# Optimization experiments

Hardware: AMD Instinct MI355X
Metric: run time of the kernel (lower is better)

Reference implementation:

```python
import jax, jax.numpy as jnp
import numpy as np

C = 256
D = C // 8  # query/key channels


def setup_inputs() -> dict:
    key = jax.random.key(0)
    ks = jax.random.split(key, 7)
    x = jax.random.normal(ks[0], (4, C, 64, 64), dtype=jnp.float32)
    s1 = 1.0 / np.sqrt(C)
    w1 = jax.random.normal(ks[1], (D, C), dtype=jnp.float32) * s1
    b1 = jax.random.normal(ks[2], (D,), dtype=jnp.float32) * 0.01
    w2 = jax.random.normal(ks[3], (D, C), dtype=jnp.float32) * s1
    b2 = jax.random.normal(ks[4], (D,), dtype=jnp.float32) * 0.01
    w3 = jax.random.normal(ks[5], (C, C), dtype=jnp.float32) * s1
    b3 = jax.random.normal(ks[6], (C,), dtype=jnp.float32) * 0.01
    return {"x": x, "w1": w1, "b1": b1, "w2": w2, "b2": b2, "w3": w3, "b3": b3}


def reference(x, w1, b1, w2, b2, w3, b3):
    B, Cc, W, H = x.shape
    N = W * H
    xf = x.reshape(B, Cc, N)  # [B, C, N] flattened spatial
    # 1x1 convs are per-pixel linear maps over channels
    q = jnp.einsum('dc,bcn->bnd', w1, xf) + b1  # [B, N, D]
    k = jnp.einsum('dc,bcn->bdn', w2, xf) + b2[:, None]  # [B, D, N]
    v = jnp.einsum('oc,bcn->bon', w3, xf) + b3[:, None]  # [B, C, N]
    energy = jnp.einsum('bnd,bdm->bnm', q, k)  # [B, N, N]
    attn = jax.nn.softmax(energy, axis=-1)
    out = jnp.einsum('bcm,bnm->bcn', v, attn)  # bmm(V, attn^T)
    out = out.reshape(B, Cc, W, H) + x
    return out
```

## Files before the change

### kernel.cpp

```cpp
#include <hip/hip_runtime.h>
#include <hip/hip_fp16.h>

typedef _Float16 half8 __attribute__((ext_vector_type(8)));
typedef _Float16 half2v __attribute__((ext_vector_type(2)));
typedef float f32x16 __attribute__((ext_vector_type(16)));
typedef float f32x4v __attribute__((ext_vector_type(4)));

#define MFMA16(A, B, C) __builtin_amdgcn_mfma_f32_32x32x16_f16((A), (B), (C), 0, 0, 0)

__device__ __forceinline__ f32x16 fzero16() {
  f32x16 z;
#pragma unroll
  for (int i = 0; i < 16; ++i) z[i] = 0.0f;
  return z;
}

struct HiLo { _Float16 hi, lo; };
__device__ __forceinline__ HiLo split1(float f) {
  HiLo r;
  r.hi = (_Float16)f;
  r.lo = (_Float16)(f - (float)r.hi);
  return r;
}

__global__ __launch_bounds__(256) void wprep_kernel(
    const float* __restrict__ w1, const float* __restrict__ w2,
    const float* __restrict__ w3,
    _Float16* __restrict__ w1p, _Float16* __restrict__ w2p,
    _Float16* __restrict__ w3p)
{
  const int t = threadIdx.x;
  const int blk = blockIdx.x;
  if (blk < 8) {
    const int cot = blk;
    for (int e = t; e < 8192; e += 256) {
      const int j = e & 7, l = (e >> 3) & 63, cs = e >> 9;
      const int lr = l & 31, h = l >> 5;
      const int row = cot * 32 + lr;
      const int col = cs * 16 + 4 * h + (j & 3) + 8 * (j >> 2);
      const HiLo s = split1(w3[row * 256 + col]);
      const int idx = ((cot * 16 + cs) * 64 + l) * 8 + j;
      w3p[idx] = s.hi;
      w3p[65536 + idx] = s.lo;
    }
  } else {
    for (int e = t; e < 8192; e += 256) {
      const int j = e & 7, l = (e >> 3) & 63, cs = e >> 9;
      const int lr = l & 31, h = l >> 5;
      const int col = cs * 16 + 4 * h + (j & 3) + 8 * (j >> 2);
      const HiLo s1 = split1(w1[lr * 256 + col]);
      const HiLo s2 = split1(w2[lr * 256 + col]);
      const int idx = (cs * 64 + l) * 8 + j;
      w1p[idx] = s1.hi; w1p[8192 + idx] = s1.lo;
      w2p[idx] = s2.hi; w2p[8192 + idx] = s2.lo;
    }
  }
}

__global__ __launch_bounds__(256) void qk_proj_kernel(
    const float* __restrict__ x,
    const _Float16* __restrict__ w1p, const float* __restrict__ b1,
    const _Float16* __restrict__ w2p, const float* __restrict__ b2,
    _Float16* __restrict__ qb, _Float16* __restrict__ kb)
{
  __shared__ f32x4v red[4][2][4][64];
  const int t = threadIdx.x, w = t >> 6, l = t & 63;
  const int lr = l & 31, h = l >> 5;
  const int b = blockIdx.x >> 7;
  const int rt = blockIdx.x & 127;
  const float* xb = x + (size_t)b * 256 * 4096 + rt * 32 + lr;

  f32x16 accq = fzero16(), acck = fzero16();

  for (int cs = w * 4; cs < w * 4 + 4; ++cs) {
    const int c0 = cs * 16 + 4 * h;
    half8 xh, xl;
#pragma unroll
    for (int j = 0; j < 8; ++j) {
      const int c = c0 + (j & 3) + 8 * (j >> 2);
      const HiLo s = split1(xb[(size_t)c * 4096]);
      xh[j] = s.hi; xl[j] = s.lo;
    }
    const half8 w1h = *(const half8*)&w1p[(cs * 64 + l) * 8];
    const half8 w1l = *(const half8*)&w1p[8192 + (cs * 64 + l) * 8];
    const half8 w2h = *(const half8*)&w2p[(cs * 64 + l) * 8];
    const half8 w2l = *(const half8*)&w2p[8192 + (cs * 64 + l) * 8];
    accq = MFMA16(w1h, xh, accq);
    accq = MFMA16(w1h, xl, accq);
    accq = MFMA16(w1l, xh, accq);
    acck = MFMA16(w2h, xh, acck);
    acck = MFMA16(w2h, xl, acck);
    acck = MFMA16(w2l, xh, acck);
  }

#pragma unroll
  for (int i4 = 0; i4 < 4; ++i4) {
    f32x4v q4, k4;
#pragma unroll
    for (int c = 0; c < 4; ++c) { q4[c] = accq[4 * i4 + c]; k4[c] = acck[4 * i4 + c]; }
    red[w][0][i4][l] = q4;
    red[w][1][i4][l] = k4;
  }
  __syncthreads();
  if (w < 2) {
    _Float16* dst = (w == 0) ? qb : kb;
    const float* bias = (w == 0) ? b1 : b2;
    f32x16 tot;
#pragma unroll
    for (int i4 = 0; i4 < 4; ++i4) {
      f32x4v v = red[0][w][i4][l];
      v += red[1][w][i4][l];
      v += red[2][w][i4][l];
      v += red[3][w][i4][l];
#pragma unroll
      for (int c = 0; c < 4; ++c) tot[4 * i4 + c] = v[c];
    }
#pragma unroll
    for (int ds = 0; ds < 2; ++ds) {
      half8 ph;
#pragma unroll
      for (int j = 0; j < 8; ++j) {
        const int d = 16 * ds + 4 * h + (j & 3) + 8 * (j >> 2);
        ph[j] = (_Float16)(tot[8 * ds + j] + bias[d]);
      }
      *(half8*)&dst[((((size_t)b * 128 + rt) * 2 + ds) * 64 + l) * 8] = ph;
    }
  }
}

__global__ __launch_bounds__(256) void v_proj_kernel(
    const float* __restrict__ x, const _Float16* __restrict__ w3p,
    const float* __restrict__ b3, _Float16* __restrict__ vb)
{
  const int t = threadIdx.x, w = t >> 6, l = t & 63;
  const int lr = l & 31, h = l >> 5;
  const int b = blockIdx.x >> 7;
  const int nt = blockIdx.x & 127;
  const float* xb = x + (size_t)b * 256 * 4096 + nt * 32 + lr;
  const int cot0 = w * 2, cot1 = w * 2 + 1;

  f32x16 acc0 = fzero16(), acc1 = fzero16();

  for (int cs = 0; cs < 16; ++cs) {
    const int c0 = cs * 16 + 4 * h;
    half8 xh, xl;
#pragma unroll
    for (int j = 0; j < 8; ++j) {
      const int c = c0 + (j & 3) + 8 * (j >> 2);
      const HiLo s = split1(xb[(size_t)c * 4096]);
      xh[j] = s.hi; xl[j] = s.lo;
    }
    const half8 wh0 = *(const half8*)&w3p[((cot0 * 16 + cs) * 64 + l) * 8];
    const half8 wl0 = *(const half8*)&w3p[65536 + ((cot0 * 16 + cs) * 64 + l) * 8];
    const half8 wh1 = *(const half8*)&w3p[((cot1 * 16 + cs) * 64 + l) * 8];
    const half8 wl1 = *(const half8*)&w3p[65536 + ((cot1 * 16 + cs) * 64 + l) * 8];
    acc0 = MFMA16(xh, wh0, acc0);
    acc0 = MFMA16(xl, wh0, acc0);
    acc0 = MFMA16(xh, wl0, acc0);
    acc1 = MFMA16(xh, wh1, acc1);
    acc1 = MFMA16(xl, wh1, acc1);
    acc1 = MFMA16(xh, wl1, acc1);
  }

  const float bv0 = b3[cot0 * 32 + lr];
  const float bv1 = b3[cot1 * 32 + lr];
#pragma unroll
  for (int hfq = 0; hfq < 2; ++hfq) {
    half8 p0, p1;
#pragma unroll
    for (int j = 0; j < 8; ++j) {
      p0[j] = (_Float16)(acc0[8 * hfq + j] + bv0);
      p1[j] = (_Float16)(acc1[8 * hfq + j] + bv1);
    }
    const int ms = nt * 2 + hfq;
    *(half8*)&vb[((((size_t)b * 256 + ms) * 8 + cot0) * 64 + l) * 8] = p0;
    *(half8*)&vb[((((size_t)b * 256 + ms) * 8 + cot1) * 64 + l) * 8] = p1;
  }
}

__global__ __launch_bounds__(512) void rowmax_kernel(
    const _Float16* __restrict__ qb, const _Float16* __restrict__ kb,
    float* __restrict__ Mrow)
{
  __shared__ float red[2][8][32];
  const int t = threadIdx.x, w = t >> 6, l = t & 63;
  const int bid = blockIdx.x;
  const int xcd = bid & 7;
  const int b = xcd >> 1;
  const int sp = ((bid >> 3) << 1) | (xcd & 1);
  const int sl0 = sp * 2, sl1 = sp * 2 + 1;
  const _Float16* qp0 = qb + ((((size_t)b * 128 + sl0) * 2) * 64 + l) * 8;
  const _Float16* qp1 = qb + ((((size_t)b * 128 + sl1) * 2) * 64 + l) * 8;
  const half8 q00 = *(const half8*)qp0;
  const half8 q01 = *(const half8*)(qp0 + 512);
  const half8 q10 = *(const half8*)qp1;
  const half8 q11 = *(const half8*)(qp1 + 512);
  float vm0 = -3.0e38f, vm1 = -3.0e38f;
  for (int mt = w * 16; mt < w * 16 + 16; ++mt) {
    const _Float16* kp = kb + ((((size_t)b * 128 + mt) * 2) * 64 + l) * 8;
    const half8 k0 = *(const half8*)kp;
    const half8 k1 = *(const half8*)(kp + 512);
    f32x16 s0 = fzero16();
    s0 = MFMA16(k0, q00, s0);
    s0 = MFMA16(k1, q01, s0);
    f32x16 s1 = fzero16();
    s1 = MFMA16(k0, q10, s1);
    s1 = MFMA16(k1, q11, s1);
#pragma unroll
    for (int i = 0; i < 16; ++i) {
      vm0 = fmaxf(vm0, s0[i]);
      vm1 = fmaxf(vm1, s1[i]);
    }
  }
  vm0 = fmaxf(vm0, __shfl_xor(vm0, 32));
  vm1 = fmaxf(vm1, __shfl_xor(vm1, 32));
  if (l < 32) { red[0][w][l] = vm0; red[1][w][l] = vm1; }
  __syncthreads();
  if (t < 64) {
    const int slab = t >> 5, r = t & 31;
    float m = red[slab][0][r];
#pragma unroll
    for (int ww = 1; ww < 8; ++ww) m = fmaxf(m, red[slab][ww][r]);
    Mrow[(size_t)b * 4096 + (sp * 2 + slab) * 32 + r] = m;
  }
}

__global__ __launch_bounds__(512, 2) void attn_kernel(
    const _Float16* __restrict__ qb, const _Float16* __restrict__ kb,
    const _Float16* __restrict__ vb, const float* __restrict__ Mrow,
    const float* __restrict__ x, float* __restrict__ out)
{
  __shared__ __align__(16) _Float16 Plds[2][2][8][64][8];
  __shared__ float Lred[2][4][32];
  const int t = threadIdx.x, w = t >> 6, l = t & 63;
  const int lr = l & 31, h = l >> 5;
  const int bid = blockIdx.x;
  const int xcd = bid & 7;
  const int b = xcd >> 1;
  const int rg = ((bid >> 3) << 1) | (xcd & 1);
  const int sw = w >> 2;
  const int kq = w & 3;

  const _Float16* kbase = kb + (size_t)b * 131072 + (size_t)l * 8;
  const _Float16* vbase = vb + (size_t)b * 1048576 + (size_t)w * 512 + (size_t)l * 8;

#define KF(it, ds) (*(const half8*)(kbase + ((size_t)(((it) * 4 + kq) * 2 + (ds))) * 512))
#define VF(it, ks) (*(const half8*)(vbase + ((size_t)(((it) * 8 + (ks)) * 8)) * 512))

  const int rt32q = rg * 2 + sw;
  const _Float16* qp = qb + (((size_t)b * 128 + rt32q) * 2 * 64 + l) * 8;
  const half8 qf0 = *(const half8*)qp;
  const half8 qf1 = *(const half8*)(qp + 512);
  const float LOG2E = 1.44269504088896340736f;
  const float Mr = Mrow[(size_t)b * 4096 + rt32q * 32 + lr];
  const float nM2 = -Mr * LOG2E;

  f32x16 acc0 = fzero16(), acc1 = fzero16();
  float Lacc = 0.f;
  half8 va[8], vn[8];
  half8 ka0, ka1, kb0_, kb1_;

#define EXPPACK(S, BUF)                                                        \
  {                                                                            \
    float pvv[16];                                                             \
    float ls = 0.f;                                                            \
    _Pragma("unroll") for (int i = 0; i < 16; ++i) {                           \
      pvv[i] = exp2f(fmaf((S)[i], LOG2E, nM2)); ls += pvv[i];                  \
    }                                                                          \
    Lacc += ls;                                                                \
    union { half8 v; half2v h2[4]; } u0, u1;                                   \
    _Pragma("unroll") for (int jj = 0; jj < 4; ++jj) {                         \
      auto a0 = __builtin_amdgcn_cvt_pkrtz(pvv[2 * jj], pvv[2 * jj + 1]);      \
      auto a1 = __builtin_amdgcn_cvt_pkrtz(pvv[8 + 2 * jj], pvv[8 + 2 * jj + 1]); \
      u0.h2[jj] = *(half2v*)&a0;                                               \
      u1.h2[jj] = *(half2v*)&a1;                                               \
    }                                                                          \
    *(half8*)&Plds[BUF][sw][kq * 2 + 0][l][0] = u0.v;                          \
    *(half8*)&Plds[BUF][sw][kq * 2 + 1][l][0] = u1.v;                          \
  }

#pragma unroll
  for (int ks = 0; ks < 8; ++ks) va[ks] = VF(0, ks);
  {
    const half8 k00 = KF(0, 0);
    const half8 k01 = KF(0, 1);
    f32x16 s0 = fzero16();
    s0 = MFMA16(k00, qf0, s0);
    s0 = MFMA16(k01, qf1, s0);
    ka0 = KF(1, 0);
    ka1 = KF(1, 1);
    EXPPACK(s0, 0)
  }
  asm volatile("s_waitcnt lgkmcnt(0)" ::: "memory");
  __builtin_amdgcn_s_barrier();
  asm volatile("" ::: "memory");

#define BODY(T, VC, VN, KC0, KC1, KN0, KN1, BUF)                               \
  {                                                                            \
    const bool more = (T) < 31;                                                \
    f32x16 s;                                                                  \
    if (more) {                                                                \
      s = fzero16();                                                           \
      s = MFMA16(KC0, qf0, s);                                                 \
      s = MFMA16(KC1, qf1, s);                                                 \
      if ((T) < 30) { KN0 = KF((T) + 2, 0); KN1 = KF((T) + 2, 1); }            \
    }                                                                          \
    _Pragma("unroll") for (int ks = 0; ks < 8; ++ks) {                         \
      const half8 pb0 = *(const half8*)&Plds[BUF][0][ks][l][0];                \
      const half8 pb1 = *(const half8*)&Plds[BUF][1][ks][l][0];                \
      acc0 = MFMA16(VC[ks], pb0, acc0);                                        \
      acc1 = MFMA16(VC[ks], pb1, acc1);                                        \
    }                                                                          \
    if (more) {                                                                \
      _Pragma("unroll") for (int ks = 0; ks < 8; ++ks)                         \
        VN[ks] = VF((T) + 1, ks);                                              \
      EXPPACK(s, (BUF) ^ 1)                                                    \
    }                                                                          \
    asm volatile("s_waitcnt lgkmcnt(0)" ::: "memory");                         \
    __builtin_amdgcn_s_barrier();                                              \
    asm volatile("" ::: "memory");                                             \
  }

  for (int it = 0; it < 32; it += 2) {
    BODY(it,     va, vn, ka0, ka1, kb0_, kb1_, 0)
    BODY(it + 1, vn, va, kb0_, kb1_, ka0, ka1, 1)
  }
#undef BODY
#undef EXPPACK
#undef KF
#undef VF

  {
    const float l2 = Lacc + __shfl_xor(Lacc, 32);
    if (l < 32) Lred[sw][kq][lr] = l2;
  }
  __syncthreads();
  const float invL0 = 1.0f / (Lred[0][0][lr] + Lred[0][1][lr] + Lred[0][2][lr] + Lred[0][3][lr]);
  const float invL1 = 1.0f / (Lred[1][0][lr] + Lred[1][1][lr] + Lred[1][2][lr] + Lred[1][3][lr]);

  const float* xb = x + (size_t)b * 1048576;
  float* ob = out + (size_t)b * 1048576;
  const int nn0 = rg * 64 + lr;
  const int nn1 = rg * 64 + 32 + lr;
#pragma unroll
  for (int reg = 0; reg < 16; ++reg) {
    const int crel = (reg & 3) + 8 * (reg >> 2) + 4 * h;
    const int cout = w * 32 + crel;
    const size_t o0 = (size_t)cout * 4096 + nn0;
    ob[o0] = acc0[reg] * invL0 + xb[o0];
    const size_t o1 = (size_t)cout * 4096 + nn1;
    ob[o1] = acc1[reg] * invL1 + xb[o1];
  }
}

extern "C" void kernel_launch(void* const* d_in, const int* in_sizes, int n_in,
                              void* d_out, int out_size, void* d_ws, size_t ws_size,
                              hipStream_t stream) {
  const float* x  = (const float*)d_in[0];
  const float* w1 = (const float*)d_in[1];
  const float* b1 = (const float*)d_in[2];
  const float* w2 = (const float*)d_in[3];
  const float* b2 = (const float*)d_in[4];
  const float* w3 = (const float*)d_in[5];
  const float* b3 = (const float*)d_in[6];
  float* out = (float*)d_out;

  char* ws = (char*)d_ws;
  _Float16* qb  = (_Float16*)(ws);
  _Float16* kb  = (_Float16*)(ws + (1u << 20));
  _Float16* vb  = (_Float16*)(ws + (2u << 20));
  float*    Mrow = (float*)(ws + (10u << 20));
  _Float16* w1p = (_Float16*)(ws + (10u << 20) + (64u << 10));
  _Float16* w2p = (_Float16*)(ws + (10u << 20) + (96u << 10));
  _Float16* w3p = (_Float16*)(ws + (10u << 20) + (128u << 10));

  hipLaunchKernelGGL(wprep_kernel, dim3(9), dim3(256), 0, stream,
                     w1, w2, w3, w1p, w2p, w3p);
  hipLaunchKernelGGL(qk_proj_kernel, dim3(512), dim3(256), 0, stream,
                     x, w1p, b1, w2p, b2, qb, kb);
  hipLaunchKernelGGL(v_proj_kernel, dim3(512), dim3(256), 0, stream,
                     x, w3p, b3, vb);
  hipLaunchKernelGGL(rowmax_kernel, dim3(256), dim3(512), 0, stream, qb, kb, Mrow);
  hipLaunchKernelGGL(attn_kernel, dim3(256), dim3(512), 0, stream,
                     qb, kb, vb, Mrow, x, out);
}
```

Baseline: 88.19 us.

## Process two key tiles per barrier with doubled P buffers and MFMA priority

Restructures the attention main loop so each barrier-delimited phase handles two key tiles instead of one. The P shared-memory buffer and V register prefetch sets are doubled, halving the number of block barriers. The PV MFMA section is wrapped in s_setprio to favour matrix work, and launch bounds drop from two blocks per CU to one to allow more registers. The cost is higher register and LDS use and less occupancy, in exchange for fewer sync points and deeper prefetch.

```diff
diff --git a/kernel.cpp b/kernel.cpp
--- a/kernel.cpp
+++ b/kernel.cpp
@@ -225,12 +225,12 @@
   }
 }
 
-__global__ __launch_bounds__(512, 2) void attn_kernel(
+__global__ __launch_bounds__(512, 1) void attn_kernel(
     const _Float16* __restrict__ qb, const _Float16* __restrict__ kb,
     const _Float16* __restrict__ vb, const float* __restrict__ Mrow,
     const float* __restrict__ x, float* __restrict__ out)
 {
-  __shared__ __align__(16) _Float16 Plds[2][2][8][64][8];
+  __shared__ __align__(16) _Float16 Plds[2][2][2][8][64][8];
   __shared__ float Lred[2][4][32];
   const int t = threadIdx.x, w = t >> 6, l = t & 63;
   const int lr = l & 31, h = l >> 5;
@@ -244,8 +244,8 @@
   const _Float16* kbase = kb + (size_t)b * 131072 + (size_t)l * 8;
   const _Float16* vbase = vb + (size_t)b * 1048576 + (size_t)w * 512 + (size_t)l * 8;
 
-#define KF(it, ds) (*(const half8*)(kbase + ((size_t)(((it) * 4 + kq) * 2 + (ds))) * 512))
-#define VF(it, ks) (*(const half8*)(vbase + ((size_t)(((it) * 8 + (ks)) * 8)) * 512))
+#define KF(kt, ds) (*(const half8*)(kbase + ((size_t)(((kt) * 4 + kq) * 2 + (ds))) * 512))
+#define VF(kt, ks) (*(const half8*)(vbase + ((size_t)(((kt) * 8 + (ks)) * 8)) * 512))
 
   const int rt32q = rg * 2 + sw;
   const _Float16* qp = qb + (((size_t)b * 128 + rt32q) * 2 * 64 + l) * 8;
@@ -257,10 +257,10 @@
 
   f32x16 acc0 = fzero16(), acc1 = fzero16();
   float Lacc = 0.f;
-  half8 va[8], vn[8];
+  half8 va0[8], va1[8];
   half8 ka0, ka1, kb0_, kb1_;
 
-#define EXPPACK(S, BUF)                                                        \
+#define EXPPACK(S, BUF, TI)                                                    \
   {                                                                            \
     float pvv[16];                                                             \
     float ls = 0.f;                                                            \
@@ -275,57 +275,81 @@
       u0.h2[jj] = *(half2v*)&a0;                                               \
       u1.h2[jj] = *(half2v*)&a1;                                               \
     }                                                                          \
-    *(half8*)&Plds[BUF][sw][kq * 2 + 0][l][0] = u0.v;                          \
-    *(half8*)&Plds[BUF][sw][kq * 2 + 1][l][0] = u1.v;                          \
-  }
-
-#pragma unroll
-  for (int ks = 0; ks < 8; ++ks) va[ks] = VF(0, ks);
+    *(half8*)&Plds[BUF][TI][sw][kq * 2 + 0][l][0] = u0.v;                      \
+    *(half8*)&Plds[BUF][TI][sw][kq * 2 + 1][l][0] = u1.v;                      \
+  }
+
+#define PVC(CB, TI, VA)                                                        \
+  {                                                                            \
+    __builtin_amdgcn_s_setprio(1);                                             \
+    _Pragma("unroll") for (int ks = 0; ks < 8; ++ks) {                         \
+      const half8 pb0 = *(const half8*)&Plds[CB][TI][0][ks][l][0];             \
+      const half8 pb1 = *(const half8*)&Plds[CB][TI][1][ks][l][0];             \
+      acc0 = MFMA16(VA[ks], pb0, acc0);                                        \
+      acc1 = MFMA16(VA[ks], pb1, acc1);                                        \
+    }                                                                          \
+    __builtin_amdgcn_s_setprio(0);                                             \
+  }
+
+#pragma unroll
+  for (int ks = 0; ks < 8; ++ks) va0[ks] = VF(0, ks);
+#pragma unroll
+  for (int ks = 0; ks < 8; ++ks) va1[ks] = VF(1, ks);
   {
-    const half8 k00 = KF(0, 0);
-    const half8 k01 = KF(0, 1);
-    f32x16 s0 = fzero16();
-    s0 = MFMA16(k00, qf0, s0);
-    s0 = MFMA16(k01, qf1, s0);
-    ka0 = KF(1, 0);
-    ka1 = KF(1, 1);
-    EXPPACK(s0, 0)
+    const half8 k00 = KF(0, 0), k01 = KF(0, 1);
+    f32x16 s = fzero16();
+    s = MFMA16(k00, qf0, s);
+    s = MFMA16(k01, qf1, s);
+    ka0 = KF(2, 0); ka1 = KF(2, 1);
+    EXPPACK(s, 0, 0)
+  }
+  {
+    const half8 k10 = KF(1, 0), k11 = KF(1, 1);
+    f32x16 s = fzero16();
+    s = MFMA16(k10, qf0, s);
+    s = MFMA16(k11, qf1, s);
+    kb0_ = KF(3, 0); kb1_ = KF(3, 1);
+    EXPPACK(s, 0, 1)
   }
   asm volatile("s_waitcnt lgkmcnt(0)" ::: "memory");
   __builtin_amdgcn_s_barrier();
   asm volatile("" ::: "memory");
 
-#define BODY(T, VC, VN, KC0, KC1, KN0, KN1, BUF)                               \
-  {                                                                            \
-    const bool more = (T) < 31;                                                \
-    f32x16 s;                                                                  \
-    if (more) {                                                                \
-      s = fzero16();                                                           \
-      s = MFMA16(KC0, qf0, s);                                                 \
-      s = MFMA16(KC1, qf1, s);                                                 \
-      if ((T) < 30) { KN0 = KF((T) + 2, 0); KN1 = KF((T) + 2, 1); }            \
-    }                                                                          \
-    _Pragma("unroll") for (int ks = 0; ks < 8; ++ks) {                         \
-      const half8 pb0 = *(const half8*)&Plds[BUF][0][ks][l][0];                \
-      const half8 pb1 = *(const half8*)&Plds[BUF][1][ks][l][0];                \
-      acc0 = MFMA16(VC[ks], pb0, acc0);                                        \
-      acc1 = MFMA16(VC[ks], pb1, acc1);                                        \
-    }                                                                          \
-    if (more) {                                                                \
-      _Pragma("unroll") for (int ks = 0; ks < 8; ++ks)                         \
-        VN[ks] = VF((T) + 1, ks);                                              \
-      EXPPACK(s, (BUF) ^ 1)                                                    \
-    }                                                                          \
-    asm volatile("s_waitcnt lgkmcnt(0)" ::: "memory");                         \
-    __builtin_amdgcn_s_barrier();                                              \
-    asm volatile("" ::: "memory");                                             \
-  }
-
-  for (int it = 0; it < 32; it += 2) {
-    BODY(it,     va, vn, ka0, ka1, kb0_, kb1_, 0)
-    BODY(it + 1, vn, va, kb0_, kb1_, ka0, ka1, 1)
-  }
-#undef BODY
+  for (int P = 0; P < 16; ++P) {
+    const int CB = P & 1, PB = CB ^ 1;
+    const int p0 = 2 * P + 2, p1 = 2 * P + 3;
+
+    if (p0 < 32) {
+      f32x16 s = fzero16();
+      s = MFMA16(ka0, qf0, s);
+      s = MFMA16(ka1, qf1, s);
+      if (p0 + 2 < 32) { ka0 = KF(p0 + 2, 0); ka1 = KF(p0 + 2, 1); }
+      EXPPACK(s, PB, 0)
+    }
+    PVC(CB, 0, va0)
+    if (p0 < 32) {
+#pragma unroll
+      for (int ks = 0; ks < 8; ++ks) va0[ks] = VF(p0, ks);
+    }
+
+    if (p1 < 32) {
+      f32x16 s = fzero16();
+      s = MFMA16(kb0_, qf0, s);
+      s = MFMA16(kb1_, qf1, s);
+      if (p1 + 2 < 32) { kb0_ = KF(p1 + 2, 0); kb1_ = KF(p1 + 2, 1); }
+      EXPPACK(s, PB, 1)
+    }
+    PVC(CB, 1, va1)
+    if (p1 < 32) {
+#pragma unroll
+      for (int ks = 0; ks < 8; ++ks) va1[ks] = VF(p1, ks);
+    }
+
+    asm volatile("s_waitcnt lgkmcnt(0)" ::: "memory");
+    __builtin_amdgcn_s_barrier();
+    asm volatile("" ::: "memory");
+  }
+#undef PVC
 #undef EXPPACK
 #undef KF
 #undef VF
```

Measured after the change: 87.86 us. Within noise of the previous version (-0.4%).
